# Optimization experiments

Hardware: AMD Instinct MI355X
Metric: run time of the kernel (lower is better)

## Reference

```python
import jax, jax.numpy as jnp
import numpy as np

TIM_SIZE, TIM_EMB = 48, 64
APP_SIZE, APP_EMB = 10000, 256
UID_SIZE, UID_EMB = 10000, 256
INPUT_SIZE = TIM_EMB + APP_EMB  # 320
S = 4096
N = S - 3  # windows of length 4


def setup_inputs() -> dict:
    key = jax.random.key(0)
    ks = jax.random.split(key, 12)
    inp = {
        "tim": jax.random.randint(ks[0], (S, 1), 0, TIM_SIZE),
        "app": jax.random.uniform(ks[1], (S, APP_SIZE), dtype=jnp.float32),
        "loc": jax.random.randint(ks[2], (S, 1), 0, 1),
        "uid": jax.random.randint(ks[3], (1,), 0, UID_SIZE),
        "ptim": jax.random.randint(ks[4], (N, 1), 0, TIM_SIZE),
        # learned parameters
        "emb_tim_w": jax.random.normal(ks[5], (TIM_SIZE, TIM_EMB), dtype=jnp.float32) * 0.02,
        "emb_uid_w": jax.random.normal(ks[6], (UID_SIZE, UID_EMB), dtype=jnp.float32) * 0.02,
        "emb_app_w": jax.random.normal(ks[7], (APP_SIZE, APP_EMB), dtype=jnp.float32) * 0.02,
        "attn_W": jax.random.uniform(ks[8], (INPUT_SIZE, 1), dtype=jnp.float32),
        "attn_b": jax.random.uniform(ks[9], (4, 1), dtype=jnp.float32),
        "attn_fc_w": jax.random.normal(ks[10], (APP_EMB, INPUT_SIZE), dtype=jnp.float32) * 0.02,
        "attn_fc_b": jnp.zeros((APP_EMB,), dtype=jnp.float32),
        "dec_w": jax.random.normal(ks[11], (APP_SIZE, APP_EMB + TIM_EMB), dtype=jnp.float32) * 0.02,
        "dec_b": jnp.zeros((APP_SIZE,), dtype=jnp.float32),
    }
    return inp


def reference(tim, app, loc, uid, ptim, emb_tim_w, emb_uid_w, emb_app_w,
              attn_W, attn_b, attn_fc_w, attn_fc_b, dec_w, dec_b):
    # embeddings (squeeze(1) in torch)
    tim_emb = emb_tim_w[tim[:, 0]]    # [S, TIM_EMB]
    ptim_emb = emb_tim_w[ptim[:, 0]]  # [N, TIM_EMB]
    # 'sum' app embedding mode: multi-hot @ table
    app_emb = app @ emb_app_w         # [S, APP_EMB]
    x = jnp.concatenate([app_emb, tim_emb], axis=1)  # [S, INPUT_SIZE]; dropout is identity at eval
    # sliding windows of length 4 (vectorizes the torch per-i loop)
    n = tim.shape[0] - 3
    idx = jnp.arange(n)[:, None] + jnp.arange(4)[None, :]  # [N, 4]
    win = x[idx]                                          # [N, 4, INPUT_SIZE]
    H = jnp.tanh(win @ attn_W + attn_b)                   # [N, 4, 1]
    Xn = H / jnp.sum(jnp.abs(H), axis=(1, 2), keepdims=True)  # L1 normalize over the window
    pooled = jnp.einsum('nf,nfd->nd', Xn[:, :, 0], win)   # [N, INPUT_SIZE]
    out = pooled @ attn_fc_w.T + attn_fc_b                # [N, APP_EMB]
    uid_emb = emb_uid_w[uid[0]]                           # [APP_EMB], broadcast = repeat
    out = out * uid_emb
    out = jnp.concatenate([out, ptim_emb], axis=1)        # [N, APP_EMB+TIM_EMB]
    score = jax.nn.sigmoid(out @ dec_w.T + dec_b)         # [N, APP_SIZE]
    return score
```

## Files before the change

kernel.cpp:

```cpp
#include <hip/hip_runtime.h>

typedef __attribute__((ext_vector_type(8))) short  bf16x8;
typedef __attribute__((ext_vector_type(8))) unsigned short u16x8;
typedef __attribute__((ext_vector_type(4))) float  f32x4;

constexpr int S    = 4096;
constexpr int NR   = 4093;
constexpr int KAPP = 10000;
constexpr int EAPP = 256;
constexpr int ETIM = 64;
constexpr int DIN  = 320;
constexpr int NDEC = 10000;
constexpr int NSK  = 8;
constexpr int KCH  = 1280;
constexpr int KPAD = NSK * KCH;
constexpr int NS   = KCH / 32;

__device__ inline unsigned short f2bf(float f) {
    unsigned u = __float_as_uint(f);
    u += 0x7fffu + ((u >> 16) & 1u);
    return (unsigned short)(u >> 16);
}
__device__ inline float bf2f(unsigned short h) {
    return __uint_as_float(((unsigned)h) << 16);
}
__device__ inline u16x8 pack8(f32x4 a, f32x4 b) {
    u16x8 v;
    v[0]=f2bf(a.x); v[1]=f2bf(a.y); v[2]=f2bf(a.z); v[3]=f2bf(a.w);
    v[4]=f2bf(b.x); v[5]=f2bf(b.y); v[6]=f2bf(b.z); v[7]=f2bf(b.w);
    return v;
}
__device__ inline bf16x8 as_bf(u16x8 v) {
    union { u16x8 u; bf16x8 b; } c; c.u = v; return c.b;
}

__global__ __launch_bounds__(256) void k_cvt_bf16(
    const float* __restrict__ in, unsigned short* __restrict__ out, int n8)
{
    int id = blockIdx.x * 256 + threadIdx.x;
    if (id >= n8) return;
    const float* p = in + (size_t)id * 8;
    f32x4 a = *reinterpret_cast<const f32x4*>(p);
    f32x4 b = *reinterpret_cast<const f32x4*>(p + 4);
    *reinterpret_cast<u16x8*>(out + (size_t)id * 8) = pack8(a, b);
}

__global__ __launch_bounds__(256) void k_bake_appw(
    const float* __restrict__ B, unsigned short* __restrict__ Bpp)
{
    __shared__ float T[64][68];
    const int kt = blockIdx.x * 64, nt = blockIdx.y * 64;
    const int tid = threadIdx.x;
    #pragma unroll
    for (int i = 0; i < 4; ++i) {
        int c = tid + (i << 8);
        int k = c >> 4, n4 = (c & 15) << 2;
        f32x4 v = {0.f, 0.f, 0.f, 0.f};
        if (kt + k < KAPP)
            v = *reinterpret_cast<const f32x4*>(&B[(size_t)(kt + k) * EAPP + nt + n4]);
        *reinterpret_cast<f32x4*>(&T[k][n4]) = v;
    }
    __syncthreads();
    #pragma unroll
    for (int i = 0; i < 2; ++i) {
        int c = tid + (i << 8);
        int ln = c & 63, lc = c >> 6;
        int t = (kt >> 5) + (lc >> 2), ck = lc & 3;
        u16x8 v;
        #pragma unroll
        for (int h = 0; h < 8; ++h) v[h] = f2bf(T[(lc << 3) + h][ln]);
        *reinterpret_cast<u16x8*>(
            &Bpp[((size_t)t * 1024 + (ck << 8) + nt + ln) * 8]) = v;
    }
}

__global__ __launch_bounds__(256) void k_embed_tim(
    const int* __restrict__ tim, const float* __restrict__ emb_tim,
    unsigned short* __restrict__ xb)
{
    int r = blockIdx.x * 4 + (threadIdx.x >> 6);
    int e = threadIdx.x & 63;
    xb[(size_t)r * DIN + EAPP + e] = f2bf(emb_tim[tim[r] * ETIM + e]);
}
__global__ __launch_bounds__(256) void k_embed_ptim(
    const int* __restrict__ ptim, const float* __restrict__ emb_tim,
    unsigned short* __restrict__ yb)
{
    int r = blockIdx.x * 4 + (threadIdx.x >> 6);
    int e = threadIdx.x & 63;
    if (r < NR) yb[(size_t)r * DIN + EAPP + e] = f2bf(emb_tim[ptim[r] * ETIM + e]);
}

__global__ __launch_bounds__(256, 4) void k_app(
    const float* __restrict__ A, const unsigned short* __restrict__ Bpp,
    float* __restrict__ part)
{
    __shared__ unsigned short Bs[2][8192];
    const int tid = threadIdx.x, lane = tid & 63, w = tid >> 6;
    const int ks = blockIdx.x, bm = blockIdx.y << 5;
    const int wc = w << 6, rl = lane & 15, kq = lane >> 4;

    const unsigned short* gB = Bpp + (size_t)(ks * NS) * 8192
                                   + ((w << 2) << 9) + lane * 8;

    f32x4 acc[2][4];
    #pragma unroll
    for (int i = 0; i < 2; ++i)
        #pragma unroll
        for (int j = 0; j < 4; ++j) acc[i][j] = (f32x4){0.f, 0.f, 0.f, 0.f};

    f32x4 a0[2][2], a1[2][2];

#define LOADA(T, DST) do {                                                      \
    const int kg_ = ks * KCH + ((T) << 5) + (kq << 3);                          \
    _Pragma("unroll")                                                           \
    for (int i = 0; i < 2; ++i) {                                               \
        f32x4 z_ = {0.f, 0.f, 0.f, 0.f};                                        \
        DST[i][0] = z_; DST[i][1] = z_;                                         \
        if (kg_ + 8 <= KAPP) {                                                  \
            const float* p_ = &A[(size_t)(bm + (i << 4) + rl) * KAPP + kg_];    \
            DST[i][0] = *reinterpret_cast<const f32x4*>(p_);                    \
            DST[i][1] = *reinterpret_cast<const f32x4*>(p_ + 4);                \
        }                                                                       \
    }                                                                           \
} while (0)

#define STAGEB(T, BUF) do {                                                     \
    const unsigned short* s_ = gB + (size_t)(T) * 8192;                         \
    _Pragma("unroll")                                                           \
    for (int q = 0; q < 4; ++q)                                                 \
        __builtin_amdgcn_global_load_lds(                                       \
            (const __attribute__((address_space(1))) void*)(s_ + (q << 9)),     \
            (__attribute__((address_space(3))) void*)(                          \
                &Bs[BUF][(((w << 2) + q) << 9)]),                               \
            16, 0, 0);                                                          \
} while (0)

#define PHASE(T, CURA, NXTA, CURB) do {                                         \
    asm volatile("s_waitcnt vmcnt(0)" ::: "memory");                            \
    __builtin_amdgcn_s_barrier();                                               \
    __builtin_amdgcn_sched_barrier(0);                                          \
    if ((T) + 1 < NS) { STAGEB((T) + 1, 1 - (CURB)); LOADA((T) + 1, NXTA); }    \
    bf16x8 af_[2], bf_[4];                                                      \
    _Pragma("unroll")                                                           \
    for (int i = 0; i < 2; ++i)                                                 \
        af_[i] = as_bf(pack8(CURA[i][0], CURA[i][1]));                          \
    _Pragma("unroll")                                                           \
    for (int j = 0; j < 4; ++j)                                                 \
        bf_[j] = *reinterpret_cast<const bf16x8*>(                              \
            &Bs[CURB][((kq << 8) + wc + (j << 4) + rl) << 3]);                  \
    _Pragma("unroll")                                                           \
    for (int i = 0; i < 2; ++i)                                                 \
        _Pragma("unroll")                                                       \
        for (int j = 0; j < 4; ++j)                                             \
            acc[i][j] = __builtin_amdgcn_mfma_f32_16x16x32_bf16(                \
                af_[i], bf_[j], acc[i][j], 0, 0, 0);                            \
} while (0)

    LOADA(0, a0); STAGEB(0, 0);
    for (int t2 = 0; t2 < NS; t2 += 2) {
        PHASE(t2,     a0, a1, 0);
        PHASE(t2 + 1, a1, a0, 1);
    }
#undef LOADA
#undef STAGEB
#undef PHASE

    float* P = part + ((size_t)ks * S + bm) * EAPP;
    const int rq = kq << 2;
    #pragma unroll
    for (int i = 0; i < 2; ++i)
        #pragma unroll
        for (int j = 0; j < 4; ++j) {
            int col = wc + j * 16 + rl;
            #pragma unroll
            for (int q = 0; q < 4; ++q)
                __builtin_nontemporal_store(acc[i][j][q],
                    &P[(size_t)(i * 16 + rq + q) * EAPP + col]);
        }
}

__global__ __launch_bounds__(256) void k_reduce_app(
    const float* __restrict__ part, unsigned short* __restrict__ xb)
{
    int id = blockIdx.x * 256 + threadIdx.x;
    int row = id >> 6, c4 = (id & 63) << 2;
    f32x4 s = {0.f, 0.f, 0.f, 0.f};
    #pragma unroll
    for (int sl = 0; sl < NSK; ++sl) {
        f32x4 v = __builtin_nontemporal_load(reinterpret_cast<const f32x4*>(
            &part[((size_t)sl * S + row) * EAPP + c4]));
        s.x += v.x; s.y += v.y; s.z += v.z; s.w += v.w;
    }
    unsigned short* o = &xb[(size_t)row * DIN + c4];
    o[0] = f2bf(s.x); o[1] = f2bf(s.y); o[2] = f2bf(s.z); o[3] = f2bf(s.w);
}

__global__ __launch_bounds__(256) void k_score(
    const unsigned short* __restrict__ xb, const float* __restrict__ W,
    float* __restrict__ s)
{
    int wv = threadIdx.x >> 6, lane = threadIdx.x & 63;
    int m = blockIdx.x * 4 + wv;
    float sum = 0.f;
    #pragma unroll
    for (int i = 0; i < 5; ++i) {
        int k = lane + (i << 6);
        sum += bf2f(xb[(size_t)m * DIN + k]) * W[k];
    }
    #pragma unroll
    for (int off = 32; off; off >>= 1) sum += __shfl_down(sum, off);
    if (lane == 0) s[m] = sum;
}

__global__ void k_pooled(
    const unsigned short* __restrict__ xb, const float* __restrict__ s,
    const float* __restrict__ attn_b, unsigned short* __restrict__ pooledb)
{
    int n = blockIdx.x, d = threadIdx.x;
    float h[4], den = 0.f;
    #pragma unroll
    for (int f = 0; f < 4; ++f) {
        h[f] = tanhf(s[n + f] + attn_b[f]);
        den += fabsf(h[f]);
    }
    float inv = 1.f / den, p = 0.f;
    #pragma unroll
    for (int f = 0; f < 4; ++f)
        p = fmaf(h[f] * inv, bf2f(xb[(size_t)(n + f) * DIN + d]), p);
    pooledb[(size_t)n * DIN + d] = f2bf(p);
}

template<int EPI>
__global__ __launch_bounds__(256, 4) void k_nt320(
    const unsigned short* __restrict__ A, const unsigned short* __restrict__ B,
    int Nb, int Mlim,
    const float* __restrict__ bias,
    const float* __restrict__ emb_uid, const int* __restrict__ uid,
    void* __restrict__ Cout, int ldc)
{
    __shared__ unsigned short As[40 * 64 * 8];
    const int tid = threadIdx.x, lane = tid & 63, w = tid >> 6;
    const int qx = gridDim.x >> 3;
    const int swz = (blockIdx.x & 7) * qx + (blockIdx.x >> 3);
    const int nbn = (Nb + 255) >> 8;
    const int bm = (swz / nbn) << 6, bn = (swz % nbn) << 8;
    const int rl = lane & 15, kq = lane >> 4;
    const int wc = w << 6;

    {
        const int row = tid >> 2, c0 = tid & 3;
        const unsigned short* src = A + (size_t)(bm + row) * DIN;
        #pragma unroll
        for (int t = 0; t < 10; ++t) {
            int ck = c0 + (t << 2);
            *reinterpret_cast<u16x8*>(&As[((ck << 6) + row) << 3]) =
                *reinterpret_cast<const u16x8*>(src + (ck << 3));
        }
    }
    __syncthreads();

    f32x4 acc[4][4];
    #pragma unroll
    for (int i = 0; i < 4; ++i)
        #pragma unroll
        for (int j = 0; j < 4; ++j) acc[i][j] = (f32x4){0.f, 0.f, 0.f, 0.f};

    u16x8 b0[4], b1[4];
#define LOADB(DST, KSN) do {                                                    \
    const int kg_ = ((KSN) << 5) + (kq << 3);                                   \
    _Pragma("unroll")                                                           \
    for (int j = 0; j < 4; ++j) {                                               \
        int brow = bn + wc + j * 16 + rl;                                       \
        u16x8 v_ = {0,0,0,0,0,0,0,0};                                           \
        if (brow < Nb)                                                          \
            v_ = *reinterpret_cast<const u16x8*>(&B[(size_t)brow * DIN + kg_]); \
        DST[j] = v_;                                                            \
    }                                                                           \
} while (0)

#define STEPNT(BARR, KSN) do {                                                  \
    const int ckb_ = (((KSN) << 2) + kq) << 6;                                  \
    bf16x8 af_[4];                                                              \
    _Pragma("unroll")                                                           \
    for (int i = 0; i < 4; ++i)                                                 \
        af_[i] = *reinterpret_cast<const bf16x8*>(                              \
            &As[(ckb_ + i * 16 + rl) << 3]);                                    \
    _Pragma("unroll")                                                           \
    for (int i = 0; i < 4; ++i)                                                 \
        _Pragma("unroll")                                                       \
        for (int j = 0; j < 4; ++j)                                             \
            acc[i][j] = __builtin_amdgcn_mfma_f32_16x16x32_bf16(                \
                af_[i], as_bf(BARR[j]), acc[i][j], 0, 0, 0);                     \
} while (0)

    LOADB(b0, 0);
    LOADB(b1, 1);
    #pragma unroll
    for (int p = 0; p < 5; ++p) {
        STEPNT(b0, 2 * p);
        if (2 * p + 2 < 10) LOADB(b0, 2 * p + 2);
        STEPNT(b1, 2 * p + 1);
        if (2 * p + 3 < 10) LOADB(b1, 2 * p + 3);
    }
#undef LOADB
#undef STEPNT

    const int rq = kq << 2;
    if (EPI == 1) {
        unsigned short* C = (unsigned short*)Cout;
        const float* us = emb_uid + (size_t)uid[0] * EAPP;
        #pragma unroll
        for (int j = 0; j < 4; ++j) {
            int col = bn + wc + j * 16 + rl;
            if (col >= Nb) continue;
            float um = us[col], bb = bias[col];
            #pragma unroll
            for (int i = 0; i < 4; ++i)
                #pragma unroll
                for (int q = 0; q < 4; ++q) {
                    int row = bm + i * 16 + rq + q;
                    if (row < Mlim)
                        C[(size_t)row * ldc + col] = f2bf((acc[i][j][q] + bb) * um);
                }
        }
    } else {
        float* C = (float*)Cout;
        float* epi = reinterpret_cast<float*>(As);
        float bb[4];
        #pragma unroll
        for (int j = 0; j < 4; ++j) {
            int col = bn + wc + j * 16 + rl;
            bb[j] = (col < Nb) ? bias[col] : 0.f;
        }
        const int r16 = tid >> 6, c4 = (tid & 63) << 2;
        #pragma unroll
        for (int i = 0; i < 4; ++i) {
            __syncthreads();
            #pragma unroll
            for (int j = 0; j < 4; ++j) {
                int colL = wc + j * 16 + rl;
                #pragma unroll
                for (int q = 0; q < 4; ++q) {
                    float v = acc[i][j][q] + bb[j];
                    epi[(rq + q) * 260 + colL] = 1.f / (1.f + __expf(-v));
                }
            }
            __syncthreads();
            #pragma unroll
            for (int r4 = 0; r4 < 4; ++r4) {
                int rowL = (r4 << 2) + r16;
                int grow = bm + (i << 4) + rowL;
                f32x4 v = *reinterpret_cast<const f32x4*>(&epi[rowL * 260 + c4]);
                if (grow < Mlim) {
                    if (bn + 256 <= Nb) {
                        __builtin_nontemporal_store(v,
                            reinterpret_cast<f32x4*>(&C[(size_t)grow * ldc + bn + c4]));
                    } else {
                        #pragma unroll
                        for (int e = 0; e < 4; ++e)
                            if (bn + c4 + e < Nb)
                                __builtin_nontemporal_store(v[e],
                                    &C[(size_t)grow * ldc + bn + c4 + e]);
                    }
                }
            }
        }
    }
}

extern "C" void kernel_launch(void* const* d_in, const int* in_sizes, int n_in,
                              void* d_out, int out_size, void* d_ws, size_t ws_size,
                              hipStream_t stream)
{
    const int*   tim       = (const int*)  d_in[0];
    const float* app       = (const float*)d_in[1];
    const int*   uid       = (const int*)  d_in[3];
    const int*   ptim      = (const int*)  d_in[4];
    const float* emb_tim_w = (const float*)d_in[5];
    const float* emb_uid_w = (const float*)d_in[6];
    const float* emb_app_w = (const float*)d_in[7];
    const float* attn_W    = (const float*)d_in[8];
    const float* attn_b    = (const float*)d_in[9];
    const float* attn_fc_w = (const float*)d_in[10];
    const float* attn_fc_b = (const float*)d_in[11];
    const float* dec_w     = (const float*)d_in[12];
    const float* dec_b     = (const float*)d_in[13];
    float* out = (float*)d_out;

    char* w = (char*)d_ws;
    size_t o = 0;
    auto alloc = [&](size_t bytes) { char* p = w + o; o = (o + bytes + 511) & ~(size_t)511; return p; };
    unsigned short* xb      = (unsigned short*)alloc((size_t)S * DIN * 2);
    unsigned short* pooledb = (unsigned short*)alloc((size_t)S * DIN * 2);
    unsigned short* yb      = (unsigned short*)alloc((size_t)S * DIN * 2);
    float*          s       = (float*)        alloc((size_t)S * 4);
    unsigned short* Bpp     = (unsigned short*)alloc((size_t)EAPP * KPAD * 2);
    unsigned short* decb    = (unsigned short*)alloc((size_t)NDEC * DIN * 2);
    unsigned short* fcb     = (unsigned short*)alloc((size_t)EAPP * DIN * 2);
    float*          part    = (float*)        alloc((size_t)NSK * S * EAPP * 4);

    k_cvt_bf16<<<(NDEC * DIN / 8 + 255) / 256, 256, 0, stream>>>(dec_w, decb, NDEC * DIN / 8);
    k_cvt_bf16<<<(EAPP * DIN / 8 + 255) / 256, 256, 0, stream>>>(attn_fc_w, fcb, EAPP * DIN / 8);
    dim3 gT(KPAD / 64, EAPP / 64);
    k_bake_appw<<<gT, 256, 0, stream>>>(emb_app_w, Bpp);
    k_embed_tim<<<S / 4, 256, 0, stream>>>(tim, emb_tim_w, xb);

    dim3 gApp(NSK, S / 32);
    k_app<<<gApp, 256, 0, stream>>>(app, Bpp, part);
    k_reduce_app<<<S * 64 / 256, 256, 0, stream>>>(part, xb);

    k_score<<<S / 4, 256, 0, stream>>>(xb, attn_W, s);
    k_pooled<<<NR, DIN, 0, stream>>>(xb, s, attn_b, pooledb);
    k_embed_ptim<<<S / 4, 256, 0, stream>>>(ptim, emb_tim_w, yb);

    k_nt320<1><<<64, 256, 0, stream>>>(pooledb, fcb, EAPP, S,
                                       attn_fc_b, emb_uid_w, uid, yb, DIN);
    k_nt320<2><<<40 * 64, 256, 0, stream>>>(yb, decb, NDEC, NR,
                                            dec_b, nullptr, nullptr, out, NDEC);
}
```

Before: 232.7 us.

## Stage A tile through LDS with triple-buffered pipeline and move K tail to reduce

```diff
diff --git a/kernel.cpp b/kernel.cpp
--- a/kernel.cpp
+++ b/kernel.cpp
@@ -12,9 +12,10 @@
 constexpr int DIN  = 320;
 constexpr int NDEC = 10000;
 constexpr int NSK  = 8;
-constexpr int KCH  = 1280;
-constexpr int KPAD = NSK * KCH;
-constexpr int NS   = KCH / 32;
+constexpr int KCH  = 1248;
+constexpr int NS   = 39;
+constexpr int TAILK= 9984;
+constexpr int KPAD = 10240;
 
 __device__ inline unsigned short f2bf(float f) {
     unsigned u = __float_as_uint(f);
@@ -91,64 +92,51 @@
     if (r < NR) yb[(size_t)r * DIN + EAPP + e] = f2bf(emb_tim[ptim[r] * ETIM + e]);
 }
 
-__global__ __launch_bounds__(256, 4) void k_app(
+__global__ __launch_bounds__(256, 2) void k_app(
     const float* __restrict__ A, const unsigned short* __restrict__ Bpp,
     float* __restrict__ part)
 {
-    __shared__ unsigned short Bs[2][8192];
+    __shared__ float          Afs[3][1024];
+    __shared__ unsigned short Bs[3][8192];
     const int tid = threadIdx.x, lane = tid & 63, w = tid >> 6;
     const int ks = blockIdx.x, bm = blockIdx.y << 5;
     const int wc = w << 6, rl = lane & 15, kq = lane >> 4;
-
-    const unsigned short* gB = Bpp + (size_t)(ks * NS) * 8192
-                                   + ((w << 2) << 9) + lane * 8;
-
-    f32x4 acc[2][4];
-    #pragma unroll
-    for (int i = 0; i < 2; ++i)
-        #pragma unroll
-        for (int j = 0; j < 4; ++j) acc[i][j] = (f32x4){0.f, 0.f, 0.f, 0.f};
-
-    f32x4 a0[2][2], a1[2][2];
-
-#define LOADA(T, DST) do {                                                      \
-    const int kg_ = ks * KCH + ((T) << 5) + (kq << 3);                          \
-    _Pragma("unroll")                                                           \
-    for (int i = 0; i < 2; ++i) {                                               \
-        f32x4 z_ = {0.f, 0.f, 0.f, 0.f};                                        \
-        DST[i][0] = z_; DST[i][1] = z_;                                         \
-        if (kg_ + 8 <= KAPP) {                                                  \
-            const float* p_ = &A[(size_t)(bm + (i << 4) + rl) * KAPP + kg_];    \
-            DST[i][0] = *reinterpret_cast<const f32x4*>(p_);                    \
-            DST[i][1] = *reinterpret_cast<const f32x4*>(p_ + 4);                \
-        }                                                                       \
-    }                                                                           \
-} while (0)
-
-#define STAGEB(T, BUF) do {                                                     \
-    const unsigned short* s_ = gB + (size_t)(T) * 8192;                         \
+    const int k0 = ks * KCH;
+
+    const int ap = (w << 6) + lane;
+    const float* gA = A + (size_t)(bm + (ap & 31)) * KAPP + k0 + ((ap >> 5) << 2);
+    const unsigned short* gB = Bpp + ((size_t)(ks * NS) << 13) + (lane << 3);
+
+#define STAGE(T, BUF) do {                                                      \
+    __builtin_amdgcn_global_load_lds(                                           \
+        (const __attribute__((address_space(1))) void*)(gA + ((T) << 5)),       \
+        (__attribute__((address_space(3))) void*)(&Afs[BUF][w << 8]),           \
+        16, 0, 0);                                                              \
+    const unsigned short* sB_ = gB + ((size_t)(T) << 13);                       \
     _Pragma("unroll")                                                           \
     for (int q = 0; q < 4; ++q)                                                 \
         __builtin_amdgcn_global_load_lds(                                       \
-            (const __attribute__((address_space(1))) void*)(s_ + (q << 9)),     \
+            (const __attribute__((address_space(1))) void*)(sB_ +               \
+                ((((w << 2) + q)) << 9)),                                       \
             (__attribute__((address_space(3))) void*)(                          \
-                &Bs[BUF][(((w << 2) + q) << 9)]),                               \
+                &Bs[BUF][(((w << 2) + q)) << 9]),                               \
             16, 0, 0);                                                          \
 } while (0)
 
-#define PHASE(T, CURA, NXTA, CURB) do {                                         \
-    asm volatile("s_waitcnt vmcnt(0)" ::: "memory");                            \
-    __builtin_amdgcn_s_barrier();                                               \
-    __builtin_amdgcn_sched_barrier(0);                                          \
-    if ((T) + 1 < NS) { STAGEB((T) + 1, 1 - (CURB)); LOADA((T) + 1, NXTA); }    \
+#define COMPUTE(BUF) do {                                                       \
     bf16x8 af_[2], bf_[4];                                                      \
     _Pragma("unroll")                                                           \
-    for (int i = 0; i < 2; ++i)                                                 \
-        af_[i] = as_bf(pack8(CURA[i][0], CURA[i][1]));                          \
+    for (int i = 0; i < 2; ++i) {                                               \
+        f32x4 lo_ = *reinterpret_cast<const f32x4*>(                            \
+            &Afs[BUF][(((kq << 1)    ) * 32 + (i << 4) + rl) << 2]);            \
+        f32x4 hi_ = *reinterpret_cast<const f32x4*>(                            \
+            &Afs[BUF][(((kq << 1) + 1) * 32 + (i << 4) + rl) << 2]);            \
+        af_[i] = as_bf(pack8(lo_, hi_));                                        \
+    }                                                                           \
     _Pragma("unroll")                                                           \
     for (int j = 0; j < 4; ++j)                                                 \
         bf_[j] = *reinterpret_cast<const bf16x8*>(                              \
-            &Bs[CURB][((kq << 8) + wc + (j << 4) + rl) << 3]);                  \
+            &Bs[BUF][((kq << 8) + wc + (j << 4) + rl) << 3]);                   \
     _Pragma("unroll")                                                           \
     for (int i = 0; i < 2; ++i)                                                 \
         _Pragma("unroll")                                                       \
@@ -157,14 +145,34 @@
                 af_[i], bf_[j], acc[i][j], 0, 0, 0);                            \
 } while (0)
 
-    LOADA(0, a0); STAGEB(0, 0);
-    for (int t2 = 0; t2 < NS; t2 += 2) {
-        PHASE(t2,     a0, a1, 0);
-        PHASE(t2 + 1, a1, a0, 1);
-    }
-#undef LOADA
-#undef STAGEB
-#undef PHASE
+    f32x4 acc[2][4];
+    #pragma unroll
+    for (int i = 0; i < 2; ++i)
+        #pragma unroll
+        for (int j = 0; j < 4; ++j) acc[i][j] = (f32x4){0.f, 0.f, 0.f, 0.f};
+
+    STAGE(0, 0);
+    STAGE(1, 1);
+    int b0 = 0;
+    for (int t = 0; t < NS - 2; ++t) {
+        int b2 = b0 + 2; if (b2 >= 3) b2 -= 3;
+        asm volatile("s_waitcnt vmcnt(5)" ::: "memory");
+        __builtin_amdgcn_s_barrier();
+        __builtin_amdgcn_sched_barrier(0);
+        STAGE(t + 2, b2);
+        __builtin_amdgcn_sched_barrier(0);
+        COMPUTE(b0);
+        ++b0; if (b0 == 3) b0 = 0;
+    }
+    asm volatile("s_waitcnt vmcnt(5)" ::: "memory");
+    __builtin_amdgcn_s_barrier();
+    COMPUTE(b0);
+    ++b0; if (b0 == 3) b0 = 0;
+    asm volatile("s_waitcnt vmcnt(0)" ::: "memory");
+    __builtin_amdgcn_s_barrier();
+    COMPUTE(b0);
+#undef STAGE
+#undef COMPUTE
 
     float* P = part + ((size_t)ks * S + bm) * EAPP;
     const int rq = kq << 2;
@@ -181,7 +189,8 @@
 }
 
 __global__ __launch_bounds__(256) void k_reduce_app(
-    const float* __restrict__ part, unsigned short* __restrict__ xb)
+    const float* __restrict__ part, const float* __restrict__ A,
+    const unsigned short* __restrict__ Bpp, unsigned short* __restrict__ xb)
 {
     int id = blockIdx.x * 256 + threadIdx.x;
     int row = id >> 6, c4 = (id & 63) << 2;
@@ -191,6 +200,21 @@
         f32x4 v = __builtin_nontemporal_load(reinterpret_cast<const f32x4*>(
             &part[((size_t)sl * S + row) * EAPP + c4]));
         s.x += v.x; s.y += v.y; s.z += v.z; s.w += v.w;
+    }
+    #pragma unroll
+    for (int ck = 0; ck < 2; ++ck) {
+        f32x4 a0 = *reinterpret_cast<const f32x4*>(&A[(size_t)row * KAPP + TAILK + (ck << 3)]);
+        f32x4 a1 = *reinterpret_cast<const f32x4*>(&A[(size_t)row * KAPP + TAILK + (ck << 3) + 4]);
+        float av[8] = {a0.x, a0.y, a0.z, a0.w, a1.x, a1.y, a1.z, a1.w};
+        #pragma unroll
+        for (int e = 0; e < 4; ++e) {
+            u16x8 bv = *reinterpret_cast<const u16x8*>(
+                &Bpp[((size_t)(312 * 1024 + (ck << 8) + c4 + e)) * 8]);
+            float t = 0.f;
+            #pragma unroll
+            for (int h = 0; h < 8; ++h) t = fmaf(av[h], bf2f(bv[h]), t);
+            s[e] += t;
+        }
     }
     unsigned short* o = &xb[(size_t)row * DIN + c4];
     o[0] = f2bf(s.x); o[1] = f2bf(s.y); o[2] = f2bf(s.z); o[3] = f2bf(s.w);
@@ -408,7 +432,7 @@
 
     dim3 gApp(NSK, S / 32);
     k_app<<<gApp, 256, 0, stream>>>(app, Bpp, part);
-    k_reduce_app<<<S * 64 / 256, 256, 0, stream>>>(part, xb);
+    k_reduce_app<<<S * 64 / 256, 256, 0, stream>>>(part, app, Bpp, xb);
 
     k_score<<<S / 4, 256, 0, stream>>>(xb, attn_W, s);
     k_pooled<<<NR, DIN, 0, stream>>>(xb, s, attn_b, pooledb);
```

Result: faster. 221.4 us (-4.8%).
